# Performance work log

Hardware: AMD Instinct MI355X
Metric: run time of the kernel (lower is better)

## Reference

```python
import jax, jax.numpy as jnp
import numpy as np

N, L, CS, CZ, CH, H = 1, 768, 384, 128, 32, 12
EPS = 1e-5


def _layernorm(x, w, b):
    m = jnp.mean(x, axis=-1, keepdims=True)
    v = jnp.mean((x - m) ** 2, axis=-1, keepdims=True)
    return (x - m) * jax.lax.rsqrt(v + EPS) * w + b


def setup_inputs() -> dict:
    key = jax.random.key(0)
    ks = jax.random.split(key, 12)
    scale = 0.02
    return {
        "s": jax.random.normal(ks[0], (N, L, CS), jnp.float32),
        "z": jax.random.normal(ks[1], (N, L, L, CZ), jnp.float32),
        "ln_s_w": jnp.ones((CS,), jnp.float32),
        "ln_s_b": jnp.zeros((CS,), jnp.float32),
        "ln_z_w": jnp.ones((CZ,), jnp.float32),
        "ln_z_b": jnp.zeros((CZ,), jnp.float32),
        "w_z": jax.random.normal(ks[2], (H, CZ), jnp.float32) * scale,   # pair-bias proj (no bias)
        "w_q": jax.random.normal(ks[3], (H * CH, CS), jnp.float32) * scale,
        "w_k": jax.random.normal(ks[4], (H * CH, CS), jnp.float32) * scale,
        "w_v": jax.random.normal(ks[5], (H * CH, CS), jnp.float32) * scale,
        "w_g": jax.random.normal(ks[6], (H * CH, CS), jnp.float32) * scale,
        "b_g": jnp.zeros((H * CH,), jnp.float32),
        "w_o": jax.random.normal(ks[7], (CS, H * CH), jnp.float32) * scale,
        "b_o": jnp.zeros((CS,), jnp.float32),
    }


def reference(s, z, ln_s_w, ln_s_b, ln_z_w, ln_z_b, w_z, w_q, w_k, w_v, w_g, b_g, w_o, b_o):
    s_n = _layernorm(s, ln_s_w, ln_s_b)            # [N,L,CS]
    z_n = _layernorm(z, ln_z_w, ln_z_b)            # [N,L,L,CZ]
    # pair bias: Linear(c_z -> H, bias=False), then permute to [N,H,L,L]
    bias = jnp.einsum("nijc,hc->nhij", z_n, w_z)   # [N,H,L,L]
    # AF2-style gated MHA on s
    q = jnp.einsum("nlc,dc->nld", s_n, w_q).reshape(N, L, H, CH) * (CH ** -0.5)
    k = jnp.einsum("nlc,dc->nld", s_n, w_k).reshape(N, L, H, CH)
    v = jnp.einsum("nlc,dc->nld", s_n, w_v).reshape(N, L, H, CH)
    logits = jnp.einsum("nqhc,nkhc->nhqk", q, k) + bias
    a = jax.nn.softmax(logits, axis=-1)
    o = jnp.einsum("nhqk,nkhc->nqhc", a, v).reshape(N, L, H * CH)
    g = jax.nn.sigmoid(jnp.einsum("nlc,dc->nld", s_n, w_g) + b_g)
    o = o * g
    return jnp.einsum("nld,cd->nlc", o, w_o) + b_o  # [N,L,CS]
```

## Files before the change

kernel.cpp:

```cpp
#include <hip/hip_runtime.h>
#include <hip/hip_bf16.h>
#include <cstddef>

#define L_ 768
#define CS_ 384
#define CZ_ 128
#define CH_ 32
#define H_ 12
#define LL_ (L_*L_)
#define EPS_ 1e-5f

typedef float f4 __attribute__((ext_vector_type(4)));
typedef float f2 __attribute__((ext_vector_type(2)));

__global__ void prep_kernel(const float* __restrict__ lnzw, const float* __restrict__ lnzb,
                            const float* __restrict__ wz,
                            float* __restrict__ ww, float* __restrict__ sumww,
                            float* __restrict__ bb) {
    int t = threadIdx.x;
    int h = t >> 4;
    int c0 = (t & 15) * 8;
    if (h < H_) {
        float sw = 0.f, sb = 0.f;
        #pragma unroll
        for (int c = c0; c < c0 + 8; ++c) {
            float wv = lnzw[c] * wz[h*CZ_ + c];
            ww[h*CZ_ + c] = wv;
            sw += wv;
            sb += lnzb[c] * wz[h*CZ_ + c];
        }
        #pragma unroll
        for (int off = 8; off; off >>= 1) {
            sw += __shfl_xor(sw, off);
            sb += __shfl_xor(sb, off);
        }
        if ((t & 15) == 0) { sumww[h] = sw; bb[h] = sb; }
    }
}

__global__ __launch_bounds__(256) void bias_kernel(const float* __restrict__ z,
        const float* __restrict__ ww, const float* __restrict__ sumww,
        const float* __restrict__ bb, float* __restrict__ bias) {
    __shared__ float lw[H_*CZ_];
    __shared__ float lsw[H_];
    __shared__ float lbb[H_];

    const int t = threadIdx.x;
    const size_t row = (size_t)blockIdx.x * 256 + t;
    const f4* zr = (const f4*)(z + row * CZ_);

    for (int i = t; i < H_*CZ_; i += 256) lw[i] = ww[i];
    if (t < H_) { lsw[t] = sumww[t]; lbb[t] = bb[t]; }

    float acc[H_];
    #pragma unroll
    for (int h = 0; h < H_; ++h) acc[h] = 0.f;
    float sm = 0.f, sq = 0.f;

    __syncthreads();

    #pragma unroll 1
    for (int c = 0; c < 4; ++c) {
        f4 st[8];
        #pragma unroll
        for (int j = 0; j < 8; ++j) st[j] = zr[c*8 + j];
        #pragma unroll
        for (int j = 0; j < 8; ++j) {
            f4 zv = st[j];
            sm += zv.x + zv.y + zv.z + zv.w;
            sq += zv.x*zv.x + zv.y*zv.y + zv.z*zv.z + zv.w*zv.w;
            const int cb = c*32 + j*4;
            #pragma unroll
            for (int h = 0; h < H_; ++h) {
                f4 wv = *(const f4*)&lw[h*CZ_ + cb];
                acc[h] += zv.x*wv.x + zv.y*wv.y + zv.z*wv.z + zv.w*wv.w;
            }
        }
    }

    float m = sm * (1.f/CZ_);
    float r = rsqrtf(sq*(1.f/CZ_) - m*m + EPS_);
    #pragma unroll
    for (int h = 0; h < H_; ++h)
        bias[(size_t)h*LL_ + row] = r*(acc[h] - m*lsw[h]) + lbb[h];
}

__global__ void sln_kernel(const float* __restrict__ s, const float* __restrict__ w,
                           const float* __restrict__ b, float* __restrict__ sn) {
    int row = blockIdx.x;
    int lane = threadIdx.x;
    float x[6];
    float sum = 0.f, sum2 = 0.f;
    #pragma unroll
    for (int j = 0; j < 6; ++j) {
        x[j] = s[row*CS_ + lane + j*64];
        sum += x[j]; sum2 += x[j]*x[j];
    }
    #pragma unroll
    for (int off = 32; off; off >>= 1) {
        sum  += __shfl_xor(sum,  off);
        sum2 += __shfl_xor(sum2, off);
    }
    float m = sum * (1.f/CS_);
    float r = rsqrtf(sum2*(1.f/CS_) - m*m + EPS_);
    #pragma unroll
    for (int j = 0; j < 6; ++j) {
        int c = lane + j*64;
        sn[row*CS_ + c] = (x[j]-m)*r*w[c] + b[c];
    }
}

__global__ __launch_bounds__(256) void qkvg_kernel(const float* __restrict__ sn,
        const float* __restrict__ wq, const float* __restrict__ wk,
        const float* __restrict__ wv, const float* __restrict__ wg,
        const float* __restrict__ bg,
        float* __restrict__ qb, float* __restrict__ kb,
        float* __restrict__ vb, float* __restrict__ gb) {
    __shared__ float As[16][68];
    __shared__ float Bs[16][68];
    int m0 = blockIdx.x * 64;
    int n0 = blockIdx.y * 64;
    int sel = n0 / 384;
    const float* W = (sel==0) ? wq : (sel==1) ? wk : (sel==2) ? wv : wg;
    float* C       = (sel==0) ? qb : (sel==1) ? kb : (sel==2) ? vb : gb;
    int ncol0 = n0 - sel*384;

    int t  = threadIdx.x;
    int lr = t >> 2;
    int lc = (t & 3) * 4;
    int ty = t >> 4;
    int tx = t & 15;

    float acc[4][4] = {};
    for (int k0 = 0; k0 < CS_; k0 += 16) {
        float4 av = *(const float4*)(sn + (size_t)(m0 + lr)*CS_ + k0 + lc);
        float4 bv = *(const float4*)(W  + (size_t)(ncol0 + lr)*CS_ + k0 + lc);
        As[lc+0][lr] = av.x; As[lc+1][lr] = av.y; As[lc+2][lr] = av.z; As[lc+3][lr] = av.w;
        Bs[lc+0][lr] = bv.x; Bs[lc+1][lr] = bv.y; Bs[lc+2][lr] = bv.z; Bs[lc+3][lr] = bv.w;
        __syncthreads();
        #pragma unroll
        for (int kk = 0; kk < 16; ++kk) {
            float4 a4 = *(const float4*)&As[kk][ty*4];
            float4 b4 = *(const float4*)&Bs[kk][tx*4];
            float a[4] = {a4.x,a4.y,a4.z,a4.w};
            float bb_[4] = {b4.x,b4.y,b4.z,b4.w};
            #pragma unroll
            for (int i = 0; i < 4; ++i)
                #pragma unroll
                for (int j = 0; j < 4; ++j)
                    acc[i][j] += a[i]*bb_[j];
        }
        __syncthreads();
    }
    #pragma unroll
    for (int i = 0; i < 4; ++i) {
        int row = m0 + ty*4 + i;
        #pragma unroll
        for (int j = 0; j < 4; ++j) {
            int col = ncol0 + tx*4 + j;
            float v = acc[i][j];
            if (sel == 0) v *= 0.17677669529663687f;
            if (sel == 3) v = 1.f/(1.f + __expf(-(v + bg[col])));
            C[(size_t)row*CS_ + col] = v;
        }
    }
}

#define QT_ 8
__global__ __launch_bounds__(256) void attn_kernel(const float* __restrict__ qb,
        const float* __restrict__ kb, const float* __restrict__ vb,
        const float* __restrict__ gb, const float* __restrict__ bias,
        float* __restrict__ og) {
    __shared__ float Sm[QT_][772];
    __shared__ float KVt[CH_][136];
    int h  = blockIdx.x;
    int q0 = blockIdx.y * QT_;
    int t  = threadIdx.x;

    int tq = t >> 5;
    int tk = t & 31;

    float qreg[CH_];
    {
        const float4* qsrc = (const float4*)(qb + (size_t)(q0 + tq)*CS_ + h*CH_);
        #pragma unroll
        for (int i = 0; i < 8; ++i) {
            float4 qv = qsrc[i];
            qreg[i*4+0]=qv.x; qreg[i*4+1]=qv.y; qreg[i*4+2]=qv.z; qreg[i*4+3]=qv.w;
        }
    }

    for (int kt = 0; kt < L_; kt += 128) {
        #pragma unroll
        for (int r2 = 0; r2 < 4; ++r2) {
            int row = (t >> 3) + 32*r2;
            int c   = (t & 7) * 4;
            f4 kv = *(const f4*)(kb + (size_t)(kt+row)*CS_ + h*CH_ + c);
            KVt[c+0][row]=kv.x; KVt[c+1][row]=kv.y; KVt[c+2][row]=kv.z; KVt[c+3][row]=kv.w;
        }
        __syncthreads();
        f4 sacc = {0,0,0,0};
        #pragma unroll
        for (int c = 0; c < CH_; ++c) {
            f4 kv4 = *(const f4*)&KVt[c][tk*4];
            sacc.x += qreg[c]*kv4.x;
            sacc.y += qreg[c]*kv4.y;
            sacc.z += qreg[c]*kv4.z;
            sacc.w += qreg[c]*kv4.w;
        }
        f4 bv = *(const f4*)(bias + (size_t)h*LL_ + (size_t)(q0+tq)*L_ + kt + tk*4);
        *(f4*)&Sm[tq][kt + tk*4] = sacc + bv;
        __syncthreads();
    }

    {
        float mx = -1e30f;
        for (int k = tk; k < L_; k += 32) mx = fmaxf(mx, Sm[tq][k]);
        #pragma unroll
        for (int off = 16; off; off >>= 1) mx = fmaxf(mx, __shfl_xor(mx, off));
        float ssum = 0.f;
        for (int k = tk; k < L_; k += 32) {
            float e = __expf(Sm[tq][k] - mx);
            Sm[tq][k] = e;
            ssum += e;
        }
        #pragma unroll
        for (int off = 16; off; off >>= 1) ssum += __shfl_xor(ssum, off);
        float inv = 1.f/ssum;
        for (int k = tk; k < L_; k += 32) Sm[tq][k] *= inv;
        __syncthreads();
    }

    {
        float o = 0.f;
        for (int kt = 0; kt < L_; kt += 128) {
            #pragma unroll
            for (int r2 = 0; r2 < 4; ++r2) {
                int row = (t >> 3) + 32*r2;
                int c   = (t & 7) * 4;
                f4 vv = *(const f4*)(vb + (size_t)(kt+row)*CS_ + h*CH_ + c);
                KVt[c+0][row]=vv.x; KVt[c+1][row]=vv.y; KVt[c+2][row]=vv.z; KVt[c+3][row]=vv.w;
            }
            __syncthreads();
            #pragma unroll
            for (int j4 = 0; j4 < 32; ++j4) {
                f4 pv = *(const f4*)&Sm[tq][kt + j4*4];
                f4 va = *(const f4*)&KVt[tk][j4*4];
                o += pv.x*va.x + pv.y*va.y + pv.z*va.z + pv.w*va.w;
            }
            __syncthreads();
        }
        int row = q0 + tq;
        int c   = h*CH_ + tk;
        og[(size_t)row*CS_ + c] = o * gb[(size_t)row*CS_ + c];
    }
}

__global__ __launch_bounds__(256) void outproj_kernel(const float* __restrict__ og,
        const float* __restrict__ wo, const float* __restrict__ bo,
        float* __restrict__ out) {
    __shared__ float As[16][36];
    __shared__ float Bs[16][36];
    int m0 = blockIdx.x * 32;
    int n0 = blockIdx.y * 32;
    int t  = threadIdx.x;
    int lr = t >> 3;
    int lc = (t & 7) * 2;
    int ty = t >> 4;
    int tx = t & 15;
    float acc[2][2] = {};
    for (int k0 = 0; k0 < CS_; k0 += 16) {
        f2 av = *(const f2*)(og + (size_t)(m0 + lr)*CS_ + k0 + lc);
        f2 bv = *(const f2*)(wo + (size_t)(n0 + lr)*CS_ + k0 + lc);
        As[lc+0][lr] = av.x; As[lc+1][lr] = av.y;
        Bs[lc+0][lr] = bv.x; Bs[lc+1][lr] = bv.y;
        __syncthreads();
        #pragma unroll
        for (int kk = 0; kk < 16; ++kk) {
            f2 a2 = *(const f2*)&As[kk][ty*2];
            f2 b2 = *(const f2*)&Bs[kk][tx*2];
            acc[0][0] += a2.x*b2.x;
            acc[0][1] += a2.x*b2.y;
            acc[1][0] += a2.y*b2.x;
            acc[1][1] += a2.y*b2.y;
        }
        __syncthreads();
    }
    #pragma unroll
    for (int i = 0; i < 2; ++i) {
        int row = m0 + ty*2 + i;
        #pragma unroll
        for (int j = 0; j < 2; ++j) {
            int col = n0 + tx*2 + j;
            out[(size_t)row*CS_ + col] = acc[i][j] + bo[col];
        }
    }
}

extern "C" void kernel_launch(void* const* d_in, const int* in_sizes, int n_in,
                              void* d_out, int out_size, void* d_ws, size_t ws_size,
                              hipStream_t stream) {
    const float* s      = (const float*)d_in[0];
    const float* z      = (const float*)d_in[1];
    const float* ln_s_w = (const float*)d_in[2];
    const float* ln_s_b = (const float*)d_in[3];
    const float* ln_z_w = (const float*)d_in[4];
    const float* ln_z_b = (const float*)d_in[5];
    const float* w_z    = (const float*)d_in[6];
    const float* w_q    = (const float*)d_in[7];
    const float* w_k    = (const float*)d_in[8];
    const float* w_v    = (const float*)d_in[9];
    const float* w_g    = (const float*)d_in[10];
    const float* b_g    = (const float*)d_in[11];
    const float* w_o    = (const float*)d_in[12];
    const float* b_o    = (const float*)d_in[13];
    float* out = (float*)d_out;

    float* ws    = (float*)d_ws;
    float* bias  = ws;
    float* sn    = bias + (size_t)H_*LL_;
    float* qb    = sn + (size_t)L_*CS_;
    float* kb    = qb + (size_t)L_*CS_;
    float* vb    = kb + (size_t)L_*CS_;
    float* gb    = vb + (size_t)L_*CS_;
    float* og    = gb + (size_t)L_*CS_;
    float* ww    = og + (size_t)L_*CS_;
    float* sumww = ww + (size_t)H_*CZ_;
    float* bbuf  = sumww + 16;

    hipLaunchKernelGGL(prep_kernel, dim3(1), dim3(256), 0, stream,
                       ln_z_w, ln_z_b, w_z, ww, sumww, bbuf);
    hipLaunchKernelGGL(bias_kernel, dim3(LL_/256), dim3(256), 0, stream,
                       z, ww, sumww, bbuf, bias);
    hipLaunchKernelGGL(sln_kernel, dim3(L_), dim3(64), 0, stream,
                       s, ln_s_w, ln_s_b, sn);
    hipLaunchKernelGGL(qkvg_kernel, dim3(L_/64, 1536/64), dim3(256), 0, stream,
                       sn, w_q, w_k, w_v, w_g, b_g, qb, kb, vb, gb);
    hipLaunchKernelGGL(attn_kernel, dim3(H_, L_/QT_), dim3(256), 0, stream,
                       qb, kb, vb, gb, bias, og);
    hipLaunchKernelGGL(outproj_kernel, dim3(L_/32, CS_/32), dim3(256), 0, stream,
                       og, w_o, b_o, out);
}
```

Before: 218.2 us.

## Split bias projection across threads with register-resident weights and shuffle reductions

```diff
diff --git a/kernel.cpp b/kernel.cpp
--- a/kernel.cpp
+++ b/kernel.cpp
@@ -41,48 +41,53 @@
 __global__ __launch_bounds__(256) void bias_kernel(const float* __restrict__ z,
         const float* __restrict__ ww, const float* __restrict__ sumww,
         const float* __restrict__ bb, float* __restrict__ bias) {
-    __shared__ float lw[H_*CZ_];
-    __shared__ float lsw[H_];
-    __shared__ float lbb[H_];
-
-    const int t = threadIdx.x;
-    const size_t row = (size_t)blockIdx.x * 256 + t;
-    const f4* zr = (const f4*)(z + row * CZ_);
-
-    for (int i = t; i < H_*CZ_; i += 256) lw[i] = ww[i];
-    if (t < H_) { lsw[t] = sumww[t]; lbb[t] = bb[t]; }
-
-    float acc[H_];
-    #pragma unroll
-    for (int h = 0; h < H_; ++h) acc[h] = 0.f;
-    float sm = 0.f, sq = 0.f;
-
-    __syncthreads();
+    const int t  = threadIdx.x;
+    const int c4 = t & 3;
+    const int hq = (t >> 2) & 3;
+    const int rw = t >> 4;
+    const size_t row0 = (size_t)blockIdx.x * 256;
+
+    f4 w[3][8];
+    #pragma unroll
+    for (int hh = 0; hh < 3; ++hh)
+        #pragma unroll
+        for (int j = 0; j < 8; ++j)
+            w[hh][j] = *(const f4*)(ww + (hq*3 + hh)*CZ_ + c4*32 + j*4);
+    const int sh = hq*3 + (c4 < 3 ? c4 : 2);
+    const float swh = sumww[sh];
+    const float bbh = bb[sh];
 
     #pragma unroll 1
-    for (int c = 0; c < 4; ++c) {
+    for (int p = 0; p < 16; ++p) {
+        const size_t row = row0 + p*16 + rw;
+        const f4* zr = (const f4*)(z + row*CZ_ + c4*32);
+
         f4 st[8];
         #pragma unroll
-        for (int j = 0; j < 8; ++j) st[j] = zr[c*8 + j];
+        for (int j = 0; j < 8; ++j) st[j] = zr[j];
+
+        float a0 = 0.f, a1 = 0.f, a2 = 0.f, sm = 0.f, sq = 0.f;
         #pragma unroll
         for (int j = 0; j < 8; ++j) {
             f4 zv = st[j];
             sm += zv.x + zv.y + zv.z + zv.w;
             sq += zv.x*zv.x + zv.y*zv.y + zv.z*zv.z + zv.w*zv.w;
-            const int cb = c*32 + j*4;
-            #pragma unroll
-            for (int h = 0; h < H_; ++h) {
-                f4 wv = *(const f4*)&lw[h*CZ_ + cb];
-                acc[h] += zv.x*wv.x + zv.y*wv.y + zv.z*wv.z + zv.w*wv.w;
-            }
-        }
-    }
-
-    float m = sm * (1.f/CZ_);
-    float r = rsqrtf(sq*(1.f/CZ_) - m*m + EPS_);
-    #pragma unroll
-    for (int h = 0; h < H_; ++h)
-        bias[(size_t)h*LL_ + row] = r*(acc[h] - m*lsw[h]) + lbb[h];
+            a0 += zv.x*w[0][j].x + zv.y*w[0][j].y + zv.z*w[0][j].z + zv.w*w[0][j].w;
+            a1 += zv.x*w[1][j].x + zv.y*w[1][j].y + zv.z*w[1][j].z + zv.w*w[1][j].w;
+            a2 += zv.x*w[2][j].x + zv.y*w[2][j].y + zv.z*w[2][j].z + zv.w*w[2][j].w;
+        }
+        a0 += __shfl_xor(a0, 1); a0 += __shfl_xor(a0, 2);
+        a1 += __shfl_xor(a1, 1); a1 += __shfl_xor(a1, 2);
+        a2 += __shfl_xor(a2, 1); a2 += __shfl_xor(a2, 2);
+        sm += __shfl_xor(sm, 1); sm += __shfl_xor(sm, 2);
+        sq += __shfl_xor(sq, 1); sq += __shfl_xor(sq, 2);
+
+        const float m = sm * (1.f/CZ_);
+        const float r = rsqrtf(sq*(1.f/CZ_) - m*m + EPS_);
+        const float av = (c4 == 0) ? a0 : (c4 == 1) ? a1 : a2;
+        if (c4 < 3)
+            bias[(size_t)sh*LL_ + row] = r*(av - m*swh) + bbh;
+    }
 }
 
 __global__ void sln_kernel(const float* __restrict__ s, const float* __restrict__ w,
```

New measurement: 286.0 us. 1.31x slower.
